# Optimization experiments

Hardware: AMD Instinct MI355X
Metric: run time of the kernel (lower is better)

## Reference

```python
import jax, jax.numpy as jnp
import numpy as np

D_MODEL = 512; D_INNER = 1024; D_STATE = 16; DT_RANK = 32; D_CONV = 4
N_LAYERS = 2; LSPP = 7; N_ROI = 2048; HIDDEN = 4096


def layer_norm(x, g, b, eps=1e-5):
    mu = x.mean(-1, keepdims=True)
    v = ((x - mu) ** 2).mean(-1, keepdims=True)
    return (x - mu) * jax.lax.rsqrt(v + eps) * g + b


def causal_dwconv(u, w, b):
    # u: [N,L,Di], w: [Di,K] depthwise, causal left-pad K-1
    x = jnp.transpose(u, (0, 2, 1))
    out = jax.lax.conv_general_dilated(x, w[:, None, :], (1,), [(D_CONV - 1, 0)],
                                       dimension_numbers=('NCH', 'OIH', 'NCH'),
                                       feature_group_count=D_INNER)
    return jnp.transpose(out, (0, 2, 1)) + b


def selective_scan(u, dt, A, B, C):
    # u, dt: [N,L,Di]; B, C: [N,L,S]; A: [Di,S]
    def step(h, xs):
        dt_t, B_t, C_t, u_t = xs
        dA = jnp.exp(dt_t[..., None] * A)                      # [N,Di,S]
        h = dA * h + (dt_t * u_t)[..., None] * B_t[:, None, :]
        return h, jnp.einsum('nds,ns->nd', h, C_t)
    h0 = jnp.zeros((u.shape[0], D_INNER, D_STATE), u.dtype)
    xs = (jnp.moveaxis(dt, 1, 0), jnp.moveaxis(B, 1, 0),
          jnp.moveaxis(C, 1, 0), jnp.moveaxis(u, 1, 0))
    _, ys = jax.lax.scan(step, h0, xs)
    return jnp.moveaxis(ys, 0, 1)                              # [N,L,Di]


def mamba_block(h, inw, cw, cb, xpw, dtw, dtb, Alog, Dp, ow):
    # decomposed bidirectional mamba ('dbm'): shared in_proj/gate, fwd+bwd scans summed
    xz = h @ inw.T                                             # [N,L,2*Di]
    xi, z = jnp.split(xz, 2, axis=-1)
    ys = []
    for d in range(2):
        u = xi if d == 0 else jnp.flip(xi, axis=1)
        u = jax.nn.silu(causal_dwconv(u, cw[d], cb[d]))
        dbl = u @ xpw[d].T                                     # [N,L,DT_RANK+2S]
        dtr = dbl[..., :DT_RANK]
        B = dbl[..., DT_RANK:DT_RANK + D_STATE]
        C = dbl[..., DT_RANK + D_STATE:]
        dt = jax.nn.softplus(dtr @ dtw[d].T + dtb[d])
        A = -jnp.exp(Alog[d])
        yd = selective_scan(u, dt, A, B, C) + u * Dp[d]
        ys.append(yd if d == 0 else jnp.flip(yd, axis=1))
    return ((ys[0] + ys[1]) * jax.nn.silu(z)) @ ow.T


def setup_inputs() -> dict:
    key = jax.random.key(0)
    ks = iter(jax.random.split(key, 40))
    rn = lambda shape, scale: jax.random.normal(next(ks), shape, dtype=jnp.float32) * scale
    inp = {}
    inp['x_flat'] = rn((N_ROI, D_MODEL * LSPP), 1.0)
    inp['conv_a_w'] = rn((256, 512, 3), (512 * 3) ** -0.5)
    inp['conv_p_w'] = rn((256, 512, 1), 512 ** -0.5)
    inp['se_w1'] = rn((32, 512), 512 ** -0.5)
    inp['se_b1'] = jnp.zeros((32,), jnp.float32)
    inp['se_w2'] = rn((512, 32), 32 ** -0.5)
    inp['se_b2'] = jnp.zeros((512,), jnp.float32)
    inp['ln_g'] = jnp.ones((N_LAYERS, D_MODEL), jnp.float32)
    inp['ln_b'] = jnp.zeros((N_LAYERS, D_MODEL), jnp.float32)
    inp['in_proj_w'] = rn((N_LAYERS, 2 * D_INNER, D_MODEL), D_MODEL ** -0.5)
    inp['conv_w'] = rn((N_LAYERS, 2, D_INNER, D_CONV), D_CONV ** -0.5)
    inp['conv_b'] = jnp.zeros((N_LAYERS, 2, D_INNER), jnp.float32)
    inp['x_proj_w'] = rn((N_LAYERS, 2, DT_RANK + 2 * D_STATE, D_INNER), D_INNER ** -0.5)
    inp['dt_proj_w'] = rn((N_LAYERS, 2, D_INNER, DT_RANK), DT_RANK ** -0.5)
    inp['dt_proj_b'] = rn((N_LAYERS, 2, D_INNER), 0.1) - 4.0
    inp['A_log'] = jnp.log(jnp.arange(1., D_STATE + 1., dtype=jnp.float32)) * jnp.ones((N_LAYERS, 2, D_INNER, D_STATE), jnp.float32)
    inp['D_param'] = jnp.ones((N_LAYERS, 2, D_INNER), jnp.float32)
    inp['out_proj_w'] = rn((N_LAYERS, D_MODEL, D_INNER), D_INNER ** -0.5)
    inp['out_ln_g'] = jnp.ones((D_MODEL,), jnp.float32)
    inp['out_ln_b'] = jnp.zeros((D_MODEL,), jnp.float32)
    inp['mlp_w1'] = rn((HIDDEN, D_MODEL), D_MODEL ** -0.5)
    inp['mlp_b1'] = jnp.zeros((HIDDEN,), jnp.float32)
    inp['mlp_w2'] = rn((HIDDEN, HIDDEN), HIDDEN ** -0.5)
    inp['mlp_b2'] = jnp.zeros((HIDDEN,), jnp.float32)
    return inp


def reference(x_flat, conv_a_w, conv_p_w, se_w1, se_b1, se_w2, se_b2, ln_g, ln_b,
              in_proj_w, conv_w, conv_b, x_proj_w, dt_proj_w, dt_proj_b, A_log,
              D_param, out_proj_w, out_ln_g, out_ln_b, mlp_w1, mlp_b1, mlp_w2, mlp_b2):
    N = x_flat.shape[0]
    x = x_flat.reshape(N, D_MODEL, LSPP)                       # [N,512,7]
    dn = ('NCH', 'OIH', 'NCH')
    # TSSE: strided conv branch + maxpool branch, concat, SE gating; L: 7 -> 4
    a = jax.nn.relu(jax.lax.conv_general_dilated(x, conv_a_w, (2,), [(1, 1)], dimension_numbers=dn))
    p = jax.lax.reduce_window(x, -jnp.inf, jax.lax.max, (1, 1, 3), (1, 1, 2), ((0, 0), (0, 0), (1, 1)))
    p = jax.nn.relu(jax.lax.conv_general_dilated(p, conv_p_w, (1,), [(0, 0)], dimension_numbers=dn))
    y = jnp.concatenate([a, p], axis=1)                        # [N,512,4]
    s = jax.nn.sigmoid(jax.nn.relu(y.mean(-1) @ se_w1.T + se_b1) @ se_w2.T + se_b2)
    y = y * s[:, :, None]
    # Mamba backbone: 2 pre-norm residual DBM blocks (mask is all-ones -> no-op)
    h = jnp.transpose(y, (0, 2, 1))                            # [N,L,512]
    for l in range(N_LAYERS):
        h = h + mamba_block(layer_norm(h, ln_g[l], ln_b[l]), in_proj_w[l], conv_w[l],
                            conv_b[l], x_proj_w[l], dt_proj_w[l], dt_proj_b[l],
                            A_log[l], D_param[l], out_proj_w[l])
    h = layer_norm(h, out_ln_g, out_ln_b)
    feat = h.mean(1)                                           # mean pool over time
    z1 = jax.nn.relu(feat @ mlp_w1.T + mlp_b1)
    return jax.nn.relu(z1 @ mlp_w2.T + mlp_b2)                 # [N,4096]
```

## Files before the change

kernel.cpp:

```cpp
#include <hip/hip_runtime.h>
#include <hip/hip_bf16.h>

typedef __hip_bfloat16 bf16;
typedef __attribute__((ext_vector_type(8))) short s16x8;
typedef __attribute__((ext_vector_type(4))) float f32x4;

__device__ __forceinline__ float u2f(unsigned short u){
  union { unsigned int i; float f; } v; v.i = ((unsigned int)u) << 16; return v.f;
}
__device__ __forceinline__ float bfu(bf16 x){ return __bfloat162float(x); }
__device__ __forceinline__ bf16  f2b(float x){ return __float2bfloat16(x); }

__device__ __forceinline__ void gload16(const void* g, void* l){
  __builtin_amdgcn_global_load_lds(
      (const __attribute__((address_space(1))) void*)g,
      (__attribute__((address_space(3))) void*)l, 16, 0, 0);
}

__device__ __forceinline__ float wave_sum(float v){
  #pragma unroll
  for (int o = 1; o < 64; o <<= 1) v += __shfl_xor(v, o, 64);
  return v;
}

__device__ __forceinline__ ushort4 cvt4(float4 v){
  ushort4 o;
  o.x = __bfloat16_as_ushort(f2b(v.x));
  o.y = __bfloat16_as_ushort(f2b(v.y));
  o.z = __bfloat16_as_ushort(f2b(v.z));
  o.w = __bfloat16_as_ushort(f2b(v.w));
  return o;
}

__global__ __launch_bounds__(256) void prep_im2col_kernel(
    const float* __restrict__ x_flat,
    const float* __restrict__ caw, const float* __restrict__ cpw,
    const float* __restrict__ ipw, const float* __restrict__ opw,
    const float* __restrict__ xpw, const float* __restrict__ dtw,
    const float* __restrict__ alog,
    bf16* __restrict__ Aa, bf16* __restrict__ P,
    bf16* __restrict__ wa, bf16* __restrict__ wp,
    bf16* __restrict__ wbi, bf16* __restrict__ wbo,
    bf16* __restrict__ wxp, bf16* __restrict__ wdtp,
    float* __restrict__ atab)
{
  __shared__ float xs[512][8];
  const int tid = threadIdx.x;
  if (blockIdx.x < 2048){
    const int n = blockIdx.x;
    const float* xr = x_flat + (size_t)n * 3584;
    for (int i = tid; i < 3584; i += 256) xs[i / 7][i % 7] = xr[i];
    __syncthreads();
    bf16* Ar = Aa + (size_t)n * 4 * 1536;
    for (int i = tid; i < 6144; i += 256){
      int t = i / 1536, col = i - t*1536;
      int c = col / 3, kk = col - c*3;
      int p = 2*t - 1 + kk;
      float v = (p >= 0 && p < 7) ? xs[c][p] : 0.f;
      Ar[i] = f2b(v);
    }
    bf16* Pr = P + (size_t)n * 4 * 512;
    for (int i = tid; i < 2048; i += 256){
      int t = i >> 9, c = i & 511;
      int st = 2*t - 1;
      float m = -1e30f;
      #pragma unroll
      for (int k = 0; k < 3; ++k){ int p = st + k; if (p >= 0 && p < 7) m = fmaxf(m, xs[c][p]); }
      Pr[i] = f2b(m);
    }
  } else {
    for (int i = (blockIdx.x - 2048)*256 + tid; i < 1769472; i += 2048*256){
      if (i < 917504){
        int j = i;
        const float4* src; ushort4* dst;
        if (j < 98304)      { src = (const float4*)caw; dst = (ushort4*)wa; }
        else if (j < 131072){ j -= 98304;  src = (const float4*)cpw; dst = (ushort4*)wp; }
        else if (j < 655360){ j -= 131072; src = (const float4*)ipw; dst = (ushort4*)wbi; }
        else                { j -= 655360; src = (const float4*)opw; dst = (ushort4*)wbo; }
        dst[j] = cvt4(src[j]);
      } else if (i < 1441792){
        int idx = i - 917504;
        int l = idx >> 18, rem = idx & 262143, row = rem >> 10, c = rem & 1023;
        int d = row >> 7, r = row & 127;
        float v = (r < 64) ? xpw[(((size_t)l*2 + d)*64 + r)*1024 + c] : 0.f;
        wxp[idx] = f2b(v);
      } else if (i < 1703936){
        int idx = i - 1441792;
        int ld = idx >> 16, rem = idx & 65535, r = rem >> 6, cc = rem & 63;
        float v = (cc < 32) ? dtw[((size_t)ld*1024 + r)*32 + cc] : 0.f;
        wdtp[idx] = f2b(v);
      } else {
        int idx = i - 1703936;
        atab[idx] = -__expf(alog[idx]) * 1.44269504088896f;
      }
    }
  }
}

template<int ACT, int OMODE, bool HASBIAS>
__global__ __launch_bounds__(256) void mgemm_kernel(
    const bf16* __restrict__ A, const bf16* __restrict__ W,
    const float* __restrict__ bias, void* __restrict__ outp,
    int K, int ldo)
{
  __shared__ char lsA[16384];
  __shared__ char lsB[16384];
  const int tid = threadIdx.x;
  const int w = tid >> 6, l = tid & 63;
  const int nwg = gridDim.x * gridDim.y;
  const int lin = blockIdx.y * gridDim.x + blockIdx.x;
  const int cpx = nwg >> 3;
  const int swz = (lin & 7) * cpx + (lin >> 3);
  const int m0 = (swz % gridDim.x) * 128, n0 = (swz / gridDim.x) * 128;
  const int wr = w >> 1, wc = w & 1;
  const size_t ldb = (size_t)K * 2;
  const char* Ab = (const char*)A + (size_t)m0 * ldb;
  const char* Wb = (const char*)W + (size_t)n0 * ldb;

  const int srow = l >> 3;
  const int scb  = ((l & 7) ^ srow) << 4;
  const int fr = l & 15;
  const int fg = l >> 4;
  const int fsw = (fr & 7) << 4;

  f32x4 acc[4][4];
  #pragma unroll
  for (int m = 0; m < 4; ++m)
    #pragma unroll
    for (int n = 0; n < 4; ++n) acc[m][n] = (f32x4){0.f,0.f,0.f,0.f};

  const int nk = K >> 6;
  for (int kt = 0; kt < nk; ++kt){
    const char* As = Ab + (size_t)kt * 128;
    const char* Ws = Wb + (size_t)kt * 128;
    #pragma unroll
    for (int i = 0; i < 4; ++i){
      int row = (i*4 + w)*8 + srow;
      gload16(As + (size_t)row*ldb + scb, &lsA[(i*4 + w)*1024]);
    }
    #pragma unroll
    for (int i = 0; i < 4; ++i){
      int row = (i*4 + w)*8 + srow;
      gload16(Ws + (size_t)row*ldb + scb, &lsB[(i*4 + w)*1024]);
    }
    __syncthreads();

    s16x8 af[4][2], bfr[4][2];
    #pragma unroll
    for (int m = 0; m < 4; ++m){
      int row = wr*64 + m*16 + fr;
      af[m][0] = *(const s16x8*)&lsA[row*128 + (( 0 + fg*16) ^ fsw)];
      af[m][1] = *(const s16x8*)&lsA[row*128 + ((64 + fg*16) ^ fsw)];
    }
    #pragma unroll
    for (int n = 0; n < 4; ++n){
      int row = wc*64 + n*16 + fr;
      bfr[n][0] = *(const s16x8*)&lsB[row*128 + (( 0 + fg*16) ^ fsw)];
      bfr[n][1] = *(const s16x8*)&lsB[row*128 + ((64 + fg*16) ^ fsw)];
    }
    #pragma unroll
    for (int m = 0; m < 4; ++m)
      #pragma unroll
      for (int n = 0; n < 4; ++n){
        acc[m][n] = __builtin_amdgcn_mfma_f32_16x16x32_bf16(af[m][0], bfr[n][0], acc[m][n], 0, 0, 0);
        acc[m][n] = __builtin_amdgcn_mfma_f32_16x16x32_bf16(af[m][1], bfr[n][1], acc[m][n], 0, 0, 0);
      }
    __syncthreads();
  }

  const int orow0 = m0 + wr*64, ocol0 = n0 + wc*64;
  #pragma unroll
  for (int n = 0; n < 4; ++n){
    int col = ocol0 + n*16 + fr;
    float bv = HASBIAS ? bias[col] : 0.f;
    #pragma unroll
    for (int m = 0; m < 4; ++m){
      int rbase = orow0 + m*16 + fg*4;
      #pragma unroll
      for (int r = 0; r < 4; ++r){
        float v = acc[m][n][r] + bv;
        if (ACT == 1) v = fmaxf(v, 0.f);
        if (ACT == 2) v = (v > 20.f) ? v : log1pf(__expf(v));
        size_t oi = (size_t)(rbase + r) * ldo + col;
        if (OMODE == 0)      ((bf16*)outp)[oi] = f2b(v);
        else if (OMODE == 1) ((float*)outp)[oi] = v;
        else                 ((float*)outp)[oi] += v;
      }
    }
  }
}

__global__ __launch_bounds__(256) void stemgemm_kernel(
    const bf16* __restrict__ Aa, const bf16* __restrict__ wa,
    const bf16* __restrict__ Pm, const bf16* __restrict__ wp,
    float* __restrict__ h)
{
  __shared__ char lsA[16384];
  __shared__ char lsB[16384];
  const int tid = threadIdx.x;
  const int w = tid >> 6, l = tid & 63;
  const int lin = blockIdx.y * gridDim.x + blockIdx.x;
  const int swz = (lin & 7) * 32 + (lin >> 3);
  const int tm = swz & 63, ty = swz >> 6;
  const int m0 = tm * 128;
  const bf16* A;
  const bf16* W;
  int K;
  if (ty < 2){ A = Aa; W = wa + (size_t)(ty)*128*1536; K = 1536; }
  else       { A = Pm; W = wp + (size_t)(ty-2)*128*512; K = 512; }
  const int wr = w >> 1, wc = w & 1;
  const size_t ldb = (size_t)K * 2;
  const char* Ab = (const char*)A + (size_t)m0 * ldb;
  const char* Wb = (const char*)W;

  const int srow = l >> 3;
  const int scb  = ((l & 7) ^ srow) << 4;
  const int fr = l & 15;
  const int fg = l >> 4;
  const int fsw = (fr & 7) << 4;

  f32x4 acc[4][4];
  #pragma unroll
  for (int m = 0; m < 4; ++m)
    #pragma unroll
    for (int n = 0; n < 4; ++n) acc[m][n] = (f32x4){0.f,0.f,0.f,0.f};

  const int nk = K >> 6;
  for (int kt = 0; kt < nk; ++kt){
    const char* As = Ab + (size_t)kt * 128;
    const char* Ws = Wb + (size_t)kt * 128;
    #pragma unroll
    for (int i = 0; i < 4; ++i){
      int row = (i*4 + w)*8 + srow;
      gload16(As + (size_t)row*ldb + scb, &lsA[(i*4 + w)*1024]);
    }
    #pragma unroll
    for (int i = 0; i < 4; ++i){
      int row = (i*4 + w)*8 + srow;
      gload16(Ws + (size_t)row*ldb + scb, &lsB[(i*4 + w)*1024]);
    }
    __syncthreads();

    s16x8 af[4][2], bfr[4][2];
    #pragma unroll
    for (int m = 0; m < 4; ++m){
      int row = wr*64 + m*16 + fr;
      af[m][0] = *(const s16x8*)&lsA[row*128 + (( 0 + fg*16) ^ fsw)];
      af[m][1] = *(const s16x8*)&lsA[row*128 + ((64 + fg*16) ^ fsw)];
    }
    #pragma unroll
    for (int n = 0; n < 4; ++n){
      int row = wc*64 + n*16 + fr;
      bfr[n][0] = *(const s16x8*)&lsB[row*128 + (( 0 + fg*16) ^ fsw)];
      bfr[n][1] = *(const s16x8*)&lsB[row*128 + ((64 + fg*16) ^ fsw)];
    }
    #pragma unroll
    for (int m = 0; m < 4; ++m)
      #pragma unroll
      for (int n = 0; n < 4; ++n){
        acc[m][n] = __builtin_amdgcn_mfma_f32_16x16x32_bf16(af[m][0], bfr[n][0], acc[m][n], 0, 0, 0);
        acc[m][n] = __builtin_amdgcn_mfma_f32_16x16x32_bf16(af[m][1], bfr[n][1], acc[m][n], 0, 0, 0);
      }
    __syncthreads();
  }

  const int orow0 = m0 + wr*64, ocol0 = ty*128 + wc*64;
  #pragma unroll
  for (int n = 0; n < 4; ++n){
    int col = ocol0 + n*16 + fr;
    #pragma unroll
    for (int m = 0; m < 4; ++m){
      int rbase = orow0 + m*16 + fg*4;
      #pragma unroll
      for (int r = 0; r < 4; ++r)
        h[(size_t)(rbase + r)*512 + col] = fmaxf(acc[m][n][r], 0.f);
    }
  }
}

template<int ACT, int OMODE, bool HASBIAS>
__global__ __launch_bounds__(256) void mgemm128_kernel(
    const bf16* __restrict__ A, const bf16* __restrict__ W,
    const float* __restrict__ bias, void* __restrict__ outp,
    int K, int ldo)
{
  __shared__ char lsA[32768];
  __shared__ char lsB[32768];
  const int tid = threadIdx.x;
  const int w = tid >> 6, l = tid & 63;
  const int nwg = gridDim.x * gridDim.y;
  const int lin = blockIdx.y * gridDim.x + blockIdx.x;
  const int cpx = nwg >> 3;
  const int swz = (lin & 7) * cpx + (lin >> 3);
  const int m0 = (swz % gridDim.x) * 128, n0 = (swz / gridDim.x) * 128;
  const int wr = w >> 1, wc = w & 1;
  const size_t ldb = (size_t)K * 2;
  const char* Ab = (const char*)A + (size_t)m0 * ldb;
  const char* Wb = (const char*)W + (size_t)n0 * ldb;

  const int srow4 = l >> 4;
  const int slot  = l & 15;
  const int fr = l & 15;
  const int fg = l >> 4;
  const int fx = fr & 7;

  f32x4 acc[4][4];
  #pragma unroll
  for (int m = 0; m < 4; ++m)
    #pragma unroll
    for (int n = 0; n < 4; ++n) acc[m][n] = (f32x4){0.f,0.f,0.f,0.f};

  const int nk = K >> 7;
  for (int kt = 0; kt < nk; ++kt){
    const char* As = Ab + (size_t)kt * 256;
    const char* Ws = Wb + (size_t)kt * 256;
    #pragma unroll
    for (int i = 0; i < 8; ++i){
      int c = i*4 + w;
      int row = c*4 + srow4;
      int colb = (slot ^ (row & 7)) << 4;
      gload16(As + (size_t)row*ldb + colb, &lsA[c*1024]);
      gload16(Ws + (size_t)row*ldb + colb, &lsB[c*1024]);
    }
    __syncthreads();

    #pragma unroll
    for (int half = 0; half < 2; ++half){
      s16x8 af[4][2], bfr[4][2];
      #pragma unroll
      for (int m = 0; m < 4; ++m){
        int row = wr*64 + m*16 + fr;
        af[m][0] = *(const s16x8*)&lsA[row*256 + ((((half*2+0)*4 + fg) ^ fx) << 4)];
        af[m][1] = *(const s16x8*)&lsA[row*256 + ((((half*2+1)*4 + fg) ^ fx) << 4)];
      }
      #pragma unroll
      for (int n = 0; n < 4; ++n){
        int row = wc*64 + n*16 + fr;
        bfr[n][0] = *(const s16x8*)&lsB[row*256 + ((((half*2+0)*4 + fg) ^ fx) << 4)];
        bfr[n][1] = *(const s16x8*)&lsB[row*256 + ((((half*2+1)*4 + fg) ^ fx) << 4)];
      }
      #pragma unroll
      for (int m = 0; m < 4; ++m)
        #pragma unroll
        for (int n = 0; n < 4; ++n){
          acc[m][n] = __builtin_amdgcn_mfma_f32_16x16x32_bf16(af[m][0], bfr[n][0], acc[m][n], 0, 0, 0);
          acc[m][n] = __builtin_amdgcn_mfma_f32_16x16x32_bf16(af[m][1], bfr[n][1], acc[m][n], 0, 0, 0);
        }
    }
    __syncthreads();
  }

  const int orow0 = m0 + wr*64, ocol0 = n0 + wc*64;
  #pragma unroll
  for (int n = 0; n < 4; ++n){
    int col = ocol0 + n*16 + fr;
    float bv = HASBIAS ? bias[col] : 0.f;
    #pragma unroll
    for (int m = 0; m < 4; ++m){
      int rbase = orow0 + m*16 + fg*4;
      #pragma unroll
      for (int r = 0; r < 4; ++r){
        float v = acc[m][n][r] + bv;
        if (ACT == 1) v = fmaxf(v, 0.f);
        if (ACT == 2) v = (v > 20.f) ? v : log1pf(__expf(v));
        size_t oi = (size_t)(rbase + r) * ldo + col;
        if (OMODE == 0)      ((bf16*)outp)[oi] = f2b(v);
        else if (OMODE == 1) ((float*)outp)[oi] = v;
        else                 ((float*)outp)[oi] += v;
      }
    }
  }
}

__global__ __launch_bounds__(256) void bgemm_kernel(
    const bf16* __restrict__ A, const bf16* __restrict__ W,
    bf16* __restrict__ dtr_buf, float* __restrict__ dbl)
{
  __shared__ char lsA[16384];
  __shared__ char lsB[16384];
  const int tid = threadIdx.x;
  const int w = tid >> 6, l = tid & 63;
  const int nwg = gridDim.x * 2;
  const int lin = blockIdx.y * gridDim.x + blockIdx.x;
  const int cpx = nwg >> 3;
  const int swz = (lin & 7) * cpx + (lin >> 3);
  const int m0 = (swz % gridDim.x) * 128;
  const int d  = swz / gridDim.x;
  const int K = 1024;
  const int wr = w >> 1, wc = w & 1;
  const size_t ldb = (size_t)K * 2;
  const char* Ab = (const char*)(A + (size_t)d*8388608) + (size_t)m0 * ldb;
  const char* Wb = (const char*)(W + (size_t)d*131072);

  const int srow = l >> 3;
  const int scb  = ((l & 7) ^ srow) << 4;
  const int fr = l & 15;
  const int fg = l >> 4;
  const int fsw = (fr & 7) << 4;

  f32x4 acc[4][4];
  #pragma unroll
  for (int m = 0; m < 4; ++m)
    #pragma unroll
    for (int n = 0; n < 4; ++n) acc[m][n] = (f32x4){0.f,0.f,0.f,0.f};

  const int nk = K >> 6;
  for (int kt = 0; kt < nk; ++kt){
    const char* As = Ab + (size_t)kt * 128;
    const char* Ws = Wb + (size_t)kt * 128;
    #pragma unroll
    for (int i = 0; i < 4; ++i){
      int row = (i*4 + w)*8 + srow;
      gload16(As + (size_t)row*ldb + scb, &lsA[(i*4 + w)*1024]);
    }
    #pragma unroll
    for (int i = 0; i < 4; ++i){
      int row = (i*4 + w)*8 + srow;
      gload16(Ws + (size_t)row*ldb + scb, &lsB[(i*4 + w)*1024]);
    }
    __syncthreads();

    s16x8 af[4][2], bfr[4][2];
    #pragma unroll
    for (int m = 0; m < 4; ++m){
      int row = wr*64 + m*16 + fr;
      af[m][0] = *(const s16x8*)&lsA[row*128 + (( 0 + fg*16) ^ fsw)];
      af[m][1] = *(const s16x8*)&lsA[row*128 + ((64 + fg*16) ^ fsw)];
    }
    #pragma unroll
    for (int n = 0; n < 4; ++n){
      int row = wc*64 + n*16 + fr;
      bfr[n][0] = *(const s16x8*)&lsB[row*128 + (( 0 + fg*16) ^ fsw)];
      bfr[n][1] = *(const s16x8*)&lsB[row*128 + ((64 + fg*16) ^ fsw)];
    }
    #pragma unroll
    for (int m = 0; m < 4; ++m)
      #pragma unroll
      for (int n = 0; n < 4; ++n){
        acc[m][n] = __builtin_amdgcn_mfma_f32_16x16x32_bf16(af[m][0], bfr[n][0], acc[m][n], 0, 0, 0);
        acc[m][n] = __builtin_amdgcn_mfma_f32_16x16x32_bf16(af[m][1], bfr[n][1], acc[m][n], 0, 0, 0);
      }
    __syncthreads();
  }

  const int orow0 = m0 + wr*64, c0 = wc*64;
  #pragma unroll
  for (int n = 0; n < 4; ++n){
    int col = c0 + n*16 + fr;
    #pragma unroll
    for (int m = 0; m < 4; ++m){
      int rbase = orow0 + m*16 + fg*4;
      #pragma unroll
      for (int r = 0; r < 4; ++r){
        float v = acc[m][n][r];
        int row = rbase + r;
        if (col < 32)
          dtr_buf[((size_t)d*8192 + row)*64 + col] = f2b(v);
        else if (col < 64)
          dbl[(size_t)row*128 + d*64 + (col - 32)] = v;
        else if (col < 96)
          dtr_buf[((size_t)d*8192 + row)*64 + (col - 32)] = f2b(v);
      }
    }
  }
}

__global__ __launch_bounds__(256) void dtgemm_kernel(
    const bf16* __restrict__ A, const bf16* __restrict__ W2,
    const float* __restrict__ bias2, bf16* __restrict__ out2)
{
  __shared__ char lsA[16384];
  __shared__ char lsB[16384];
  const int tid = threadIdx.x;
  const int w = tid >> 6, l = tid & 63;
  const int nwg = gridDim.x * gridDim.y;
  const int lin = blockIdx.y * gridDim.x + blockIdx.x;
  const int cpx = nwg >> 3;
  const int swz = (lin & 7) * cpx + (lin >> 3);
  const int m0 = (swz % gridDim.x) * 128, n0 = (swz / gridDim.x) * 128;
  const int d  = (m0 >= 8192) ? 1 : 0;
  const int wr = w >> 1, wc = w & 1;
  const size_t ldb = 128;
  const char* Ab = (const char*)A + (size_t)m0 * ldb;
  const char* Wb = (const char*)(W2 + (size_t)d*65536) + (size_t)n0 * ldb;
  const float* bias = bias2 + d*1024;
  bf16* outp = out2 + (size_t)d*8388608;

  const int srow = l >> 3;
  const int scb  = ((l & 7) ^ srow) << 4;
  const int fr = l & 15, fg = l >> 4;
  const int fsw = (fr & 7) << 4;

  f32x4 acc[4][4];
  #pragma unroll
  for (int m = 0; m < 4; ++m)
    #pragma unroll
    for (int n = 0; n < 4; ++n) acc[m][n] = (f32x4){0.f,0.f,0.f,0.f};

  #pragma unroll
  for (int i = 0; i < 4; ++i){
    int row = (i*4 + w)*8 + srow;
    gload16(Ab + (size_t)row*ldb + scb, &lsA[(i*4 + w)*1024]);
  }
  #pragma unroll
  for (int i = 0; i < 4; ++i){
    int row = (i*4 + w)*8 + srow;
    gload16(Wb + (size_t)row*ldb + scb, &lsB[(i*4 + w)*1024]);
  }
  __syncthreads();

  s16x8 af[4][2], bfr[4][2];
  #pragma unroll
  for (int m = 0; m < 4; ++m){
    int row = wr*64 + m*16 + fr;
    af[m][0] = *(const s16x8*)&lsA[row*128 + (( 0 + fg*16) ^ fsw)];
    af[m][1] = *(const s16x8*)&lsA[row*128 + ((64 + fg*16) ^ fsw)];
  }
  #pragma unroll
  for (int n = 0; n < 4; ++n){
    int row = wc*64 + n*16 + fr;
    bfr[n][0] = *(const s16x8*)&lsB[row*128 + (( 0 + fg*16) ^ fsw)];
    bfr[n][1] = *(const s16x8*)&lsB[row*128 + ((64 + fg*16) ^ fsw)];
  }
  #pragma unroll
  for (int m = 0; m < 4; ++m)
    #pragma unroll
    for (int n = 0; n < 4; ++n){
      acc[m][n] = __builtin_amdgcn_mfma_f32_16x16x32_bf16(af[m][0], bfr[n][0], acc[m][n], 0, 0, 0);
      acc[m][n] = __builtin_amdgcn_mfma_f32_16x16x32_bf16(af[m][1], bfr[n][1], acc[m][n], 0, 0, 0);
    }

  const int orow0 = (m0 - d*8192) + wr*64, ocol0 = n0 + wc*64;
  #pragma unroll
  for (int n = 0; n < 4; ++n){
    int col = ocol0 + n*16 + fr;
    float bv = bias[col];
    #pragma unroll
    for (int m = 0; m < 4; ++m){
      int rbase = orow0 + m*16 + fg*4;
      #pragma unroll
      for (int r = 0; r < 4; ++r){
        float v = acc[m][n][r] + bv;
        v = (v > 20.f) ? v : log1pf(__expf(v));
        outp[(size_t)(rbase + r) * 1024 + col] = f2b(v);
      }
    }
  }
}

__global__ __launch_bounds__(256) void se_ln_kernel(
    const float* __restrict__ sw1, const float* __restrict__ sb1,
    const float* __restrict__ sw2, const float* __restrict__ sb2,
    const float* __restrict__ g, const float* __restrict__ b,
    float* __restrict__ h, bf16* __restrict__ hn)
{
  __shared__ float yms[512];
  __shared__ float s1s[32];
  __shared__ float sg[512];
  const int n = blockIdx.x, tid = threadIdx.x;
  float* hb = h + (size_t)n * 2048;
  for (int c = tid; c < 512; c += 256)
    yms[c] = 0.25f * (hb[c] + hb[512+c] + hb[1024+c] + hb[1536+c]);
  __syncthreads();
  {
    int o = tid >> 3, sl = tid & 7;
    const float* wr = sw1 + (size_t)o * 512 + sl*64;
    const float* ym = yms + sl*64;
    float a = 0.f;
    #pragma unroll 16
    for (int i = 0; i < 64; ++i) a += wr[i] * ym[i];
    a += __shfl_down(a, 4, 8);
    a += __shfl_down(a, 2, 8);
    a += __shfl_down(a, 1, 8);
    if (sl == 0) s1s[o] = fmaxf(a + sb1[o], 0.f);
  }
  __syncthreads();
  for (int c = tid; c < 512; c += 256){
    float a = sb2[c];
    const float* wr = sw2 + (size_t)c * 32;
    #pragma unroll
    for (int j = 0; j < 32; ++j) a += wr[j] * s1s[j];
    sg[c] = 1.f / (1.f + __expf(-a));
  }
  __syncthreads();
  const int lane = tid & 63, wv = tid >> 6;
  float* hr = hb + wv*512;
  float4 v0 = ((float4*)hr)[lane], v1 = ((float4*)hr)[lane + 64];
  int c0 = lane*4, c1 = 256 + lane*4;
  v0.x *= sg[c0+0]; v0.y *= sg[c0+1]; v0.z *= sg[c0+2]; v0.w *= sg[c0+3];
  v1.x *= sg[c1+0]; v1.y *= sg[c1+1]; v1.z *= sg[c1+2]; v1.w *= sg[c1+3];
  ((float4*)hr)[lane] = v0;
  ((float4*)hr)[lane + 64] = v1;
  float s = wave_sum(v0.x+v0.y+v0.z+v0.w + v1.x+v1.y+v1.z+v1.w);
  float mu = s * (1.f/512.f);
  float d0x=v0.x-mu, d0y=v0.y-mu, d0z=v0.z-mu, d0w=v0.w-mu;
  float d1x=v1.x-mu, d1y=v1.y-mu, d1z=v1.z-mu, d1w=v1.w-mu;
  float sq = wave_sum(d0x*d0x+d0y*d0y+d0z*d0z+d0w*d0w +
                      d1x*d1x+d1y*d1y+d1z*d1z+d1w*d1w);
  float rstd = rsqrtf(sq * (1.f/512.f) + 1e-5f);
  float4 g0 = ((const float4*)g)[lane], g1 = ((const float4*)g)[lane+64];
  float4 b0 = ((const float4*)b)[lane], b1 = ((const float4*)b)[lane+64];
  ushort4 o0, o1;
  o0.x = __bfloat16_as_ushort(f2b(d0x*rstd*g0.x + b0.x));
  o0.y = __bfloat16_as_ushort(f2b(d0y*rstd*g0.y + b0.y));
  o0.z = __bfloat16_as_ushort(f2b(d0z*rstd*g0.z + b0.z));
  o0.w = __bfloat16_as_ushort(f2b(d0w*rstd*g0.w + b0.w));
  o1.x = __bfloat16_as_ushort(f2b(d1x*rstd*g1.x + b1.x));
  o1.y = __bfloat16_as_ushort(f2b(d1y*rstd*g1.y + b1.y));
  o1.z = __bfloat16_as_ushort(f2b(d1z*rstd*g1.z + b1.z));
  o1.w = __bfloat16_as_ushort(f2b(d1w*rstd*g1.w + b1.w));
  ushort4* orow = (ushort4*)(hn + ((size_t)n*4 + wv)*512);
  orow[lane] = o0;
  orow[lane + 64] = o1;
}

__global__ __launch_bounds__(256) void ln_kernel(
    const float* __restrict__ x, const float* __restrict__ g,
    const float* __restrict__ b, bf16* __restrict__ out)
{
  const int lane = threadIdx.x & 63, wid = threadIdx.x >> 6;
  const int row = blockIdx.x*4 + wid;
  const float4* xr = (const float4*)(x + (size_t)row*512);
  float4 v0 = xr[lane], v1 = xr[lane + 64];
  float s = wave_sum(v0.x+v0.y+v0.z+v0.w + v1.x+v1.y+v1.z+v1.w);
  float mu = s * (1.f/512.f);
  float d0x=v0.x-mu, d0y=v0.y-mu, d0z=v0.z-mu, d0w=v0.w-mu;
  float d1x=v1.x-mu, d1y=v1.y-mu, d1z=v1.z-mu, d1w=v1.w-mu;
  float sq = wave_sum(d0x*d0x+d0y*d0y+d0z*d0z+d0w*d0w +
                      d1x*d1x+d1y*d1y+d1z*d1z+d1w*d1w);
  float rstd = rsqrtf(sq * (1.f/512.f) + 1e-5f);
  float4 g0 = ((const float4*)g)[lane], g1 = ((const float4*)g)[lane+64];
  float4 b0 = ((const float4*)b)[lane], b1 = ((const float4*)b)[lane+64];
  ushort4 o0, o1;
  o0.x = __bfloat16_as_ushort(f2b(d0x*rstd*g0.x + b0.x));
  o0.y = __bfloat16_as_ushort(f2b(d0y*rstd*g0.y + b0.y));
  o0.z = __bfloat16_as_ushort(f2b(d0z*rstd*g0.z + b0.z));
  o0.w = __bfloat16_as_ushort(f2b(d0w*rstd*g0.w + b0.w));
  o1.x = __bfloat16_as_ushort(f2b(d1x*rstd*g1.x + b1.x));
  o1.y = __bfloat16_as_ushort(f2b(d1y*rstd*g1.y + b1.y));
  o1.z = __bfloat16_as_ushort(f2b(d1z*rstd*g1.z + b1.z));
  o1.w = __bfloat16_as_ushort(f2b(d1w*rstd*g1.w + b1.w));
  ushort4* orow = (ushort4*)(out + (size_t)row*512);
  orow[lane] = o0;
  orow[lane + 64] = o1;
}

__global__ __launch_bounds__(256) void finalln_mlp_kernel(
    const float* __restrict__ h, const float* __restrict__ g,
    const float* __restrict__ b, bf16* __restrict__ feat,
    const float4* __restrict__ w1, const float4* __restrict__ w2,
    ushort4* __restrict__ o1, ushort4* __restrict__ o2)
{
  __shared__ float red[4];
  const int tid = threadIdx.x;
  if (blockIdx.x < 2048){
    const int n = blockIdx.x, t = tid;
    float a0 = 0.f, a1 = 0.f;
    for (int tt = 0; tt < 4; ++tt){
      const float* xr = h + ((size_t)n*4 + tt)*512;
      float v0 = xr[t], v1 = xr[t+256];
      float sv = v0 + v1;
      #pragma unroll
      for (int o = 32; o > 0; o >>= 1) sv += __shfl_down(sv, o, 64);
      int lane = tid & 63, wid = tid >> 6;
      if (lane == 0) red[wid] = sv;
      __syncthreads();
      float s = red[0] + red[1] + red[2] + red[3];
      __syncthreads();
      float mu = s * (1.f/512.f);
      float d0 = v0 - mu, d1 = v1 - mu;
      float q = d0*d0 + d1*d1;
      #pragma unroll
      for (int o = 32; o > 0; o >>= 1) q += __shfl_down(q, o, 64);
      if (lane == 0) red[wid] = q;
      __syncthreads();
      float sq = red[0] + red[1] + red[2] + red[3];
      __syncthreads();
      float rstd = rsqrtf(sq * (1.f/512.f) + 1e-5f);
      a0 += d0*rstd*g[t]     + b[t];
      a1 += d1*rstd*g[t+256] + b[t+256];
    }
    feat[(size_t)n*512 + t]       = f2b(a0 * 0.25f);
    feat[(size_t)n*512 + t + 256] = f2b(a1 * 0.25f);
  } else {
    for (int i = (blockIdx.x - 2048)*256 + tid; i < 4718592; i += 4096*256){
      if (i < 524288) o1[i] = cvt4(w1[i]);
      else            o2[i - 524288] = cvt4(w2[i - 524288]);
    }
  }
}

__global__ __launch_bounds__(256) void dwconv2_kernel(
    const bf16* __restrict__ xz, const float* __restrict__ cw,
    const float* __restrict__ cb, bf16* __restrict__ u)
{
  const int n = blockIdx.x;
  const int c4 = threadIdx.x * 4;
  ushort4 in4[4];
  #pragma unroll
  for (int t = 0; t < 4; ++t)
    in4[t] = *reinterpret_cast<const ushort4*>(&xz[((size_t)n*4 + t)*2048 + c4]);
  #pragma unroll
  for (int d = 0; d < 2; ++d){
    const float* cwd = cw + d*4096;
    const float* cbd = cb + d*1024;
    ushort4 out[4];
    #pragma unroll
    for (int j = 0; j < 4; ++j){
      float xa[4];
      #pragma unroll
      for (int t = 0; t < 4; ++t){
        int ts = d ? 3 - t : t;
        unsigned short us = j==0?in4[ts].x : j==1?in4[ts].y : j==2?in4[ts].z : in4[ts].w;
        xa[t] = u2f(us);
      }
      float4 wv = *reinterpret_cast<const float4*>(&cwd[(c4 + j)*4]);
      float bb = cbd[c4 + j];
      float o[4];
      o[0] = xa[0]*wv.w + bb;
      o[1] = xa[0]*wv.z + xa[1]*wv.w + bb;
      o[2] = xa[0]*wv.y + xa[1]*wv.z + xa[2]*wv.w + bb;
      o[3] = xa[0]*wv.x + xa[1]*wv.y + xa[2]*wv.z + xa[3]*wv.w + bb;
      #pragma unroll
      for (int t = 0; t < 4; ++t){
        float v = o[t];
        float sv = v / (1.f + __expf(-v));
        unsigned short us = __bfloat16_as_ushort(f2b(sv));
        if (j==0) out[t].x = us; else if (j==1) out[t].y = us;
        else if (j==2) out[t].z = us; else out[t].w = us;
      }
    }
    #pragma unroll
    for (int t = 0; t < 4; ++t)
      *reinterpret_cast<ushort4*>(&u[(size_t)d*8388608 + ((size_t)n*4 + t)*1024 + c4]) = out[t];
  }
}

__global__ __launch_bounds__(256) void scan2_kernel(
    const float* __restrict__ dbl, const bf16* __restrict__ dt2,
    const bf16* __restrict__ u, const bf16* __restrict__ xz,
    const float* __restrict__ Atab2, const float* __restrict__ Dp,
    bf16* __restrict__ gated)
{
  __shared__ float Bs[2][4][16], Cs[2][4][16];
  const int n = blockIdx.x, g = blockIdx.y, tid = threadIdx.x;
  {
    int t = tid >> 6, j = tid & 63;
    int d = j >> 5, jj = j & 31;
    float v = dbl[((size_t)n*4 + t)*128 + d*64 + jj];
    if (jj < 16) Bs[d][t][jj] = v; else Cs[d][t][jj-16] = v;
  }
  __syncthreads();
  const int c = g*256 + tid;
  const size_t base = (size_t)n*4*1024 + c;
  float yo0[4], yo1[4];
  float hs[16];
  {
    float A[16];
    const float4* ap = reinterpret_cast<const float4*>(Atab2 + (size_t)c*16);
    #pragma unroll
    for (int q = 0; q < 4; ++q){
      float4 v = ap[q];
      A[q*4+0]=v.x; A[q*4+1]=v.y; A[q*4+2]=v.z; A[q*4+3]=v.w;
    }
    const float Dpc = Dp[c];
    #pragma unroll
    for (int s = 0; s < 16; ++s) hs[s] = 0.f;
    #pragma unroll
    for (int t = 0; t < 4; ++t){
      float dtv = bfu(dt2[base + (size_t)t*1024]);
      float uv  = bfu(u  [base + (size_t)t*1024]);
      float du = dtv * uv;
      float yv = 0.f;
      #pragma unroll
      for (int s = 0; s < 16; ++s){
        float dA = __builtin_amdgcn_exp2f(dtv * A[s]);
        hs[s] = dA * hs[s] + du * Bs[0][t][s];
        yv += hs[s] * Cs[0][t][s];
      }
      yo0[t] = yv + uv * Dpc;
    }
  }
  {
    float A[16];
    const float4* ap = reinterpret_cast<const float4*>(Atab2 + 16384 + (size_t)c*16);
    #pragma unroll
    for (int q = 0; q < 4; ++q){
      float4 v = ap[q];
      A[q*4+0]=v.x; A[q*4+1]=v.y; A[q*4+2]=v.z; A[q*4+3]=v.w;
    }
    const float Dpc = Dp[1024 + c];
    #pragma unroll
    for (int s = 0; s < 16; ++s) hs[s] = 0.f;
    #pragma unroll
    for (int t = 0; t < 4; ++t){
      float dtv = bfu(dt2[8388608 + base + (size_t)t*1024]);
      float uv  = bfu(u  [8388608 + base + (size_t)t*1024]);
      float du = dtv * uv;
      float yv = 0.f;
      #pragma unroll
      for (int s = 0; s < 16; ++s){
        float dA = __builtin_amdgcn_exp2f(dtv * A[s]);
        hs[s] = dA * hs[s] + du * Bs[1][t][s];
        yv += hs[s] * Cs[1][t][s];
      }
      yo1[3 - t] = yv + uv * Dpc;
    }
  }
  #pragma unroll
  for (int t = 0; t < 4; ++t){
    float z = bfu(xz[(size_t)(n*4 + t)*2048 + 1024 + c]);
    float sv = z / (1.f + __expf(-z));
    gated[base + (size_t)t*1024] = f2b((yo0[t] + yo1[t]) * sv);
  }
}

extern "C" void kernel_launch(void* const* d_in, const int* in_sizes, int n_in,
                              void* d_out, int out_size, void* d_ws, size_t ws_size,
                              hipStream_t stream)
{
  const float* x_flat    = (const float*)d_in[0];
  const float* conv_a_w  = (const float*)d_in[1];
  const float* conv_p_w  = (const float*)d_in[2];
  const float* se_w1     = (const float*)d_in[3];
  const float* se_b1     = (const float*)d_in[4];
  const float* se_w2     = (const float*)d_in[5];
  const float* se_b2     = (const float*)d_in[6];
  const float* ln_g      = (const float*)d_in[7];
  const float* ln_b      = (const float*)d_in[8];
  const float* in_proj_w = (const float*)d_in[9];
  const float* conv_w    = (const float*)d_in[10];
  const float* conv_b    = (const float*)d_in[11];
  const float* x_proj_w  = (const float*)d_in[12];
  const float* dt_proj_w = (const float*)d_in[13];
  const float* dt_proj_b = (const float*)d_in[14];
  const float* A_log     = (const float*)d_in[15];
  const float* D_param   = (const float*)d_in[16];
  const float* out_proj_w= (const float*)d_in[17];
  const float* out_ln_g  = (const float*)d_in[18];
  const float* out_ln_b  = (const float*)d_in[19];
  const float* mlp_w1    = (const float*)d_in[20];
  const float* mlp_b1    = (const float*)d_in[21];
  const float* mlp_w2    = (const float*)d_in[22];
  const float* mlp_b2    = (const float*)d_in[23];

  char* ws = (char*)d_ws;
  const size_t OFF_H    = 0;
  const size_t OFF_HN   = OFF_H    + 16777216;
  const size_t OFF_XZ   = OFF_HN   + 8388608;
  const size_t OFF_U    = OFF_XZ   + 33554432;
  const size_t OFF_SCR  = OFF_U    + 33554432;
  const size_t OFF_YB   = OFF_SCR  + 25165824;
  const size_t OFF_WB   = OFF_YB   + 33554432;
  const size_t OFF_WXP  = OFF_WB   + 6291456;
  const size_t OFF_WDT  = OFF_WXP  + 1048576;
  const size_t OFF_ATAB = OFF_WDT  + 524288;

  float* h    = (float*)(ws + OFF_H);
  bf16*  hn   = (bf16*) (ws + OFF_HN);
  bf16*  xz   = (bf16*) (ws + OFF_XZ);
  bf16*  u    = (bf16*) (ws + OFF_U);
  float* dbl  = (float*)(ws + OFF_SCR);
  bf16*  dtrb = (bf16*) (ws + OFF_SCR + 4194304);
  bf16*  dt2  = (bf16*) (ws + OFF_YB);
  bf16*  feat = (bf16*) (ws + OFF_HN);
  bf16*  z1   = (bf16*) (ws + OFF_XZ);
  bf16*  wbi  = (bf16*) (ws + OFF_WB);
  bf16*  wbo  = (bf16*) (ws + OFF_WB + 4194304);
  bf16*  wxp  = (bf16*) (ws + OFF_WXP);
  bf16*  wdtp = (bf16*) (ws + OFF_WDT);
  float* Atab = (float*)(ws + OFF_ATAB);
  bf16*  wb1  = (bf16*) (ws + OFF_SCR);
  bf16*  wb2  = (bf16*) (ws + OFF_YB);
  bf16*  Aa   = (bf16*) (ws + OFF_SCR);
  bf16*  Pm   = (bf16*) (ws + OFF_YB);
  bf16*  wa   = (bf16*) (ws + OFF_YB + 8388608);
  bf16*  wp   = (bf16*) (ws + OFF_YB + 8388608 + 786432);
  float* outf = (float*)d_out;

  prep_im2col_kernel<<<4096, 256, 0, stream>>>(
      x_flat, conv_a_w, conv_p_w, in_proj_w, out_proj_w, x_proj_w, dt_proj_w,
      A_log, Aa, Pm, wa, wp, wbi, wbo, wxp, wdtp, Atab);

  stemgemm_kernel<<<dim3(64,4), 256, 0, stream>>>(Aa, wa, Pm, wp, h);

  se_ln_kernel<<<2048, 256, 0, stream>>>(
      se_w1, se_b1, se_w2, se_b2, ln_g, ln_b, h, hn);

  for (int l = 0; l < 2; ++l){
    if (l == 1)
      ln_kernel<<<2048, 256, 0, stream>>>(h, ln_g + 512, ln_b + 512, hn);
    mgemm_kernel<0,0,false><<<dim3(64,16), 256, 0, stream>>>(
        hn, wbi + (size_t)l*2048*512, nullptr, xz, 512, 2048);
    dwconv2_kernel<<<2048, 256, 0, stream>>>(
        xz, conv_w + (size_t)l*8192, conv_b + (size_t)l*2048, u);
    bgemm_kernel<<<dim3(64,2), 256, 0, stream>>>(
        u, wxp + (size_t)l*262144, dtrb, dbl);
    dtgemm_kernel<<<dim3(128,8), 256, 0, stream>>>(
        dtrb, wdtp + (size_t)l*131072, dt_proj_b + (size_t)l*2048, dt2);
    scan2_kernel<<<dim3(2048,4), 256, 0, stream>>>(
        dbl, dt2, u, xz, Atab + (size_t)l*32768, D_param + (size_t)l*2048,
        u );
    mgemm128_kernel<0,2,false><<<dim3(64,4), 256, 0, stream>>>(
        u, wbo + (size_t)l*512*1024, nullptr, h, 1024, 512);
  }

  finalln_mlp_kernel<<<6144, 256, 0, stream>>>(
      h, out_ln_g, out_ln_b, feat,
      (const float4*)mlp_w1, (const float4*)mlp_w2, (ushort4*)wb1, (ushort4*)wb2);

  mgemm128_kernel<1,0,true><<<dim3(16,32), 256, 0, stream>>>(
      feat, wb1, mlp_b1, z1, 512, 4096);
  mgemm128_kernel<1,1,true><<<dim3(16,32), 256, 0, stream>>>(
      z1, wb2, mlp_b2, outf, 4096, 4096);
}
```

Measured before the change: 636.8 us.

## Fuse depthwise causal conv and SiLU into in_proj GEMM epilogue

Adds an in_proj GEMM kernel whose epilogue applies the forward and backward causal depthwise conv plus SiLU directly on the accumulator tile and writes u for both directions. The z half goes to a separate buffer. This works because each MFMA lane holds four consecutive rows, which are the four timesteps of one ROI. It removes the standalone dwconv kernel and the round trip of the xz half to global memory. The cost is scattered 2-byte stores in the epilogue and some extra epilogue register pressure.

```diff
diff --git a/kernel.cpp b/kernel.cpp
--- a/kernel.cpp
+++ b/kernel.cpp
@@ -31,6 +31,7 @@
   o.w = __bfloat16_as_ushort(f2b(v.w));
   return o;
 }
+__device__ __forceinline__ float silu(float v){ return v / (1.f + __expf(-v)); }
 
 __global__ __launch_bounds__(256) void prep_im2col_kernel(
     const float* __restrict__ x_flat,
@@ -185,6 +186,120 @@
         if (OMODE == 0)      ((bf16*)outp)[oi] = f2b(v);
         else if (OMODE == 1) ((float*)outp)[oi] = v;
         else                 ((float*)outp)[oi] += v;
+      }
+    }
+  }
+}
+
+__global__ __launch_bounds__(256) void ipgemm_kernel(
+    const bf16* __restrict__ A, const bf16* __restrict__ W,
+    const float* __restrict__ cw, const float* __restrict__ cb,
+    bf16* __restrict__ u, bf16* __restrict__ z)
+{
+  __shared__ char lsA[16384];
+  __shared__ char lsB[16384];
+  const int tid = threadIdx.x;
+  const int w = tid >> 6, l = tid & 63;
+  const int nwg = gridDim.x * gridDim.y;
+  const int lin = blockIdx.y * gridDim.x + blockIdx.x;
+  const int cpx = nwg >> 3;
+  const int swz = (lin & 7) * cpx + (lin >> 3);
+  const int m0 = (swz % gridDim.x) * 128, n0 = (swz / gridDim.x) * 128;
+  const int wr = w >> 1, wc = w & 1;
+  const int K = 512;
+  const size_t ldb = (size_t)K * 2;
+  const char* Ab = (const char*)A + (size_t)m0 * ldb;
+  const char* Wb = (const char*)W + (size_t)n0 * ldb;
+
+  const int srow = l >> 3;
+  const int scb  = ((l & 7) ^ srow) << 4;
+  const int fr = l & 15;
+  const int fg = l >> 4;
+  const int fsw = (fr & 7) << 4;
+
+  f32x4 acc[4][4];
+  #pragma unroll
+  for (int m = 0; m < 4; ++m)
+    #pragma unroll
+    for (int n = 0; n < 4; ++n) acc[m][n] = (f32x4){0.f,0.f,0.f,0.f};
+
+  for (int kt = 0; kt < 8; ++kt){
+    const char* As = Ab + (size_t)kt * 128;
+    const char* Ws = Wb + (size_t)kt * 128;
+    #pragma unroll
+    for (int i = 0; i < 4; ++i){
+      int row = (i*4 + w)*8 + srow;
+      gload16(As + (size_t)row*ldb + scb, &lsA[(i*4 + w)*1024]);
+    }
+    #pragma unroll
+    for (int i = 0; i < 4; ++i){
+      int row = (i*4 + w)*8 + srow;
+      gload16(Ws + (size_t)row*ldb + scb, &lsB[(i*4 + w)*1024]);
+    }
+    __syncthreads();
+
+    s16x8 af[4][2], bfr[4][2];
+    #pragma unroll
+    for (int m = 0; m < 4; ++m){
+      int row = wr*64 + m*16 + fr;
+      af[m][0] = *(const s16x8*)&lsA[row*128 + (( 0 + fg*16) ^ fsw)];
+      af[m][1] = *(const s16x8*)&lsA[row*128 + ((64 + fg*16) ^ fsw)];
+    }
+    #pragma unroll
+    for (int n = 0; n < 4; ++n){
+      int row = wc*64 + n*16 + fr;
+      bfr[n][0] = *(const s16x8*)&lsB[row*128 + (( 0 + fg*16) ^ fsw)];
+      bfr[n][1] = *(const s16x8*)&lsB[row*128 + ((64 + fg*16) ^ fsw)];
+    }
+    #pragma unroll
+    for (int m = 0; m < 4; ++m)
+      #pragma unroll
+      for (int n = 0; n < 4; ++n){
+        acc[m][n] = __builtin_amdgcn_mfma_f32_16x16x32_bf16(af[m][0], bfr[n][0], acc[m][n], 0, 0, 0);
+        acc[m][n] = __builtin_amdgcn_mfma_f32_16x16x32_bf16(af[m][1], bfr[n][1], acc[m][n], 0, 0, 0);
+      }
+    __syncthreads();
+  }
+
+  const int orow0 = m0 + wr*64, ocol0 = n0 + wc*64;
+  if (ocol0 < 1024){
+    #pragma unroll
+    for (int n = 0; n < 4; ++n){
+      int col = ocol0 + n*16 + fr;
+      float4 w0 = *(const float4*)&cw[(size_t)col*4];
+      float4 w1 = *(const float4*)&cw[4096 + (size_t)col*4];
+      float b0 = cb[col], b1 = cb[1024 + col];
+      #pragma unroll
+      for (int m = 0; m < 4; ++m){
+        int rbase = orow0 + m*16 + fg*4;
+        float x0 = acc[m][n][0], x1 = acc[m][n][1];
+        float x2 = acc[m][n][2], x3 = acc[m][n][3];
+        float o0[4], o1[4];
+        o0[0] = x0*w0.w + b0;
+        o0[1] = x0*w0.z + x1*w0.w + b0;
+        o0[2] = x0*w0.y + x1*w0.z + x2*w0.w + b0;
+        o0[3] = x0*w0.x + x1*w0.y + x2*w0.z + x3*w0.w + b0;
+        o1[0] = x3*w1.w + b1;
+        o1[1] = x3*w1.z + x2*w1.w + b1;
+        o1[2] = x3*w1.y + x2*w1.z + x1*w1.w + b1;
+        o1[3] = x3*w1.x + x2*w1.y + x1*w1.z + x0*w1.w + b1;
+        #pragma unroll
+        for (int t = 0; t < 4; ++t){
+          u[(size_t)(rbase + t)*1024 + col]           = f2b(silu(o0[t]));
+          u[8388608 + (size_t)(rbase + t)*1024 + col] = f2b(silu(o1[t]));
+        }
+      }
+    }
+  } else {
+    #pragma unroll
+    for (int n = 0; n < 4; ++n){
+      int col = ocol0 - 1024 + n*16 + fr;
+      #pragma unroll
+      for (int m = 0; m < 4; ++m){
+        int rbase = orow0 + m*16 + fg*4;
+        #pragma unroll
+        for (int r = 0; r < 4; ++r)
+          z[(size_t)(rbase + r)*1024 + col] = f2b(acc[m][n][r]);
       }
     }
   }
@@ -690,55 +805,9 @@
   }
 }
 
-__global__ __launch_bounds__(256) void dwconv2_kernel(
-    const bf16* __restrict__ xz, const float* __restrict__ cw,
-    const float* __restrict__ cb, bf16* __restrict__ u)
-{
-  const int n = blockIdx.x;
-  const int c4 = threadIdx.x * 4;
-  ushort4 in4[4];
-  #pragma unroll
-  for (int t = 0; t < 4; ++t)
-    in4[t] = *reinterpret_cast<const ushort4*>(&xz[((size_t)n*4 + t)*2048 + c4]);
-  #pragma unroll
-  for (int d = 0; d < 2; ++d){
-    const float* cwd = cw + d*4096;
-    const float* cbd = cb + d*1024;
-    ushort4 out[4];
-    #pragma unroll
-    for (int j = 0; j < 4; ++j){
-      float xa[4];
-      #pragma unroll
-      for (int t = 0; t < 4; ++t){
-        int ts = d ? 3 - t : t;
-        unsigned short us = j==0?in4[ts].x : j==1?in4[ts].y : j==2?in4[ts].z : in4[ts].w;
-        xa[t] = u2f(us);
-      }
-      float4 wv = *reinterpret_cast<const float4*>(&cwd[(c4 + j)*4]);
-      float bb = cbd[c4 + j];
-      float o[4];
-      o[0] = xa[0]*wv.w + bb;
-      o[1] = xa[0]*wv.z + xa[1]*wv.w + bb;
-      o[2] = xa[0]*wv.y + xa[1]*wv.z + xa[2]*wv.w + bb;
-      o[3] = xa[0]*wv.x + xa[1]*wv.y + xa[2]*wv.z + xa[3]*wv.w + bb;
-      #pragma unroll
-      for (int t = 0; t < 4; ++t){
-        float v = o[t];
-        float sv = v / (1.f + __expf(-v));
-        unsigned short us = __bfloat16_as_ushort(f2b(sv));
-        if (j==0) out[t].x = us; else if (j==1) out[t].y = us;
-        else if (j==2) out[t].z = us; else out[t].w = us;
-      }
-    }
-    #pragma unroll
-    for (int t = 0; t < 4; ++t)
-      *reinterpret_cast<ushort4*>(&u[(size_t)d*8388608 + ((size_t)n*4 + t)*1024 + c4]) = out[t];
-  }
-}
-
 __global__ __launch_bounds__(256) void scan2_kernel(
     const float* __restrict__ dbl, const bf16* __restrict__ dt2,
-    const bf16* __restrict__ u, const bf16* __restrict__ xz,
+    const bf16* __restrict__ u, const bf16* __restrict__ z,
     const float* __restrict__ Atab2, const float* __restrict__ Dp,
     bf16* __restrict__ gated)
 {
@@ -809,8 +878,8 @@
   }
   #pragma unroll
   for (int t = 0; t < 4; ++t){
-    float z = bfu(xz[(size_t)(n*4 + t)*2048 + 1024 + c]);
-    float sv = z / (1.f + __expf(-z));
+    float zv = bfu(z[base + (size_t)t*1024]);
+    float sv = zv / (1.f + __expf(-zv));
     gated[base + (size_t)t*1024] = f2b((yo0[t] + yo1[t]) * sv);
   }
 }
@@ -858,7 +927,7 @@
 
   float* h    = (float*)(ws + OFF_H);
   bf16*  hn   = (bf16*) (ws + OFF_HN);
-  bf16*  xz   = (bf16*) (ws + OFF_XZ);
+  bf16*  z    = (bf16*) (ws + OFF_XZ);
   bf16*  u    = (bf16*) (ws + OFF_U);
   float* dbl  = (float*)(ws + OFF_SCR);
   bf16*  dtrb = (bf16*) (ws + OFF_SCR + 4194304);
@@ -890,16 +959,15 @@
   for (int l = 0; l < 2; ++l){
     if (l == 1)
       ln_kernel<<<2048, 256, 0, stream>>>(h, ln_g + 512, ln_b + 512, hn);
-    mgemm_kernel<0,0,false><<<dim3(64,16), 256, 0, stream>>>(
-        hn, wbi + (size_t)l*2048*512, nullptr, xz, 512, 2048);
-    dwconv2_kernel<<<2048, 256, 0, stream>>>(
-        xz, conv_w + (size_t)l*8192, conv_b + (size_t)l*2048, u);
+    ipgemm_kernel<<<dim3(64,16), 256, 0, stream>>>(
+        hn, wbi + (size_t)l*2048*512,
+        conv_w + (size_t)l*8192, conv_b + (size_t)l*2048, u, z);
     bgemm_kernel<<<dim3(64,2), 256, 0, stream>>>(
         u, wxp + (size_t)l*262144, dtrb, dbl);
     dtgemm_kernel<<<dim3(128,8), 256, 0, stream>>>(
         dtrb, wdtp + (size_t)l*131072, dt_proj_b + (size_t)l*2048, dt2);
     scan2_kernel<<<dim3(2048,4), 256, 0, stream>>>(
-        dbl, dt2, u, xz, Atab + (size_t)l*32768, D_param + (size_t)l*2048,
+        dbl, dt2, u, z, Atab + (size_t)l*32768, D_param + (size_t)l*2048,
         u );
     mgemm128_kernel<0,2,false><<<dim3(64,4), 256, 0, stream>>>(
         u, wbo + (size_t)l*512*1024, nullptr, h, 1024, 512);
```

Result: slower. 656.7 us (+3.1%).
